# Kernel optimization log

Hardware: AMD Instinct MI355X
Metric: run time of the kernel (lower is better)

## Reference

```python
import jax, jax.numpy as jnp
import numpy as np

NUM_NODES = 100000
EMBED_DIM = 128
COMP_DIM = 64
T = 8
NSUB = 50000


def layer_norm(x, g, b, eps=1e-5):
    mu = jnp.mean(x, axis=-1, keepdims=True)
    var = jnp.mean((x - mu) ** 2, axis=-1, keepdims=True)
    return (x - mu) * jax.lax.rsqrt(var + eps) * g + b


def setup_inputs() -> dict:
    key = jax.random.key(0)
    ks = jax.random.split(key, 12)
    D, C = EMBED_DIM, COMP_DIM
    s = lambda n: 1.0 / np.sqrt(n)
    return {
        "x": jax.random.normal(ks[0], (T * NSUB, D), dtype=jnp.float32),
        "indices": jax.random.randint(ks[1], (T, NSUB), 0, NUM_NODES, dtype=jnp.int64),
        "bd": jax.random.normal(ks[2], (NUM_NODES, D), dtype=jnp.float32),
        "ln_d_g": jnp.ones((D,), jnp.float32), "ln_d_b": jnp.zeros((D,), jnp.float32),
        "Wd1": jax.random.normal(ks[3], (D, 2 * D), jnp.float32) * s(D),
        "bd1": jnp.zeros((2 * D,), jnp.float32),
        "Wd2": jax.random.normal(ks[4], (2 * D, C), jnp.float32) * s(2 * D),
        "bd2": jnp.zeros((C,), jnp.float32),
        "ln_u_g": jnp.ones((C,), jnp.float32), "ln_u_b": jnp.zeros((C,), jnp.float32),
        "Wu1": jax.random.normal(ks[5], (C, 2 * C), jnp.float32) * s(C),
        "bu1": jnp.zeros((2 * C,), jnp.float32),
        "Wu2": jax.random.normal(ks[6], (2 * C, D), jnp.float32) * s(2 * C),
        "bu2": jnp.zeros((D,), jnp.float32),
    }


def reference(x, indices, bd, ln_d_g, ln_d_b, Wd1, bd1, Wd2, bd2,
              ln_u_g, ln_u_b, Wu1, bu1, Wu2, bu2):
    # _to_entire: per-timestep scatter-add of subnode feats into full node table
    x3 = x.reshape(T, NSUB, EMBED_DIM)  # [T, Nsub, D]
    scattered = jax.vmap(
        lambda xt, it: jax.ops.segment_sum(xt, it, num_segments=NUM_NODES)
    )(x3, indices)  # [T, num_nodes, D]
    inp = scattered + bd[None]  # ta + bd (use_bd=True)
    h = layer_norm(inp, ln_d_g, ln_d_b)
    # mlp_d: Linear -> GELU -> Dropout(eval=identity) -> Linear
    h = jax.nn.gelu(h @ Wd1 + bd1, approximate=False) @ Wd2 + bd2  # [T, num_nodes, C]
    # _from_entire: gather activated rows per timestep, then LN + mlp_u
    gathered = jax.vmap(lambda ht, it: ht[it])(h, indices)  # [T, Nsub, C]
    g = gathered.reshape(T * NSUB, COMP_DIM)
    u = layer_norm(g, ln_u_g, ln_u_b)
    out = jax.nn.gelu(u @ Wu1 + bu1, approximate=False) @ Wu2 + bu2  # [T*Nsub, D]
    return out
```

## Files before the change

kernel.cpp:

```cpp
#include <hip/hip_runtime.h>
#include <math.h>

#define NN 100000
#define DD 128
#define CC 64
#define TT 8
#define NS 50000
#define G8 8
#define MAXS 391
#define MAXS_B 196
#define T1MAX (G8 * MAXS)
#define T2MAX (G8 * MAXS_B)
#define L2CAP 25000

typedef __attribute__((ext_vector_type(4))) float f32x4;
typedef __attribute__((ext_vector_type(8))) short bf16x8;
typedef unsigned short ushort_t;

__device__ __forceinline__ short f2bf(float f) {
    union { float f; unsigned u; } v; v.f = f;
    unsigned r = v.u + 0x7fffu + ((v.u >> 16) & 1u);
    return (short)(r >> 16);
}
__device__ __forceinline__ unsigned pk_bf16(float lo, float hi) {
    unsigned r;
    asm("v_cvt_pk_bf16_f32 %0, %1, %2" : "=v"(r) : "v"(lo), "v"(hi));
    return r;
}
__device__ __forceinline__ float gelu(float x) {
    float t = x + 0.044715f * x * x * x;
    return x / (1.0f + __expf(-1.5957691216f * t));
}

__global__ void prep_all(const float* __restrict__ Wd1, const float* __restrict__ Wd2,
                         const float* __restrict__ Wu1, const float* __restrict__ Wu2,
                         short* __restrict__ pW1, short* __restrict__ pW2,
                         short* __restrict__ pW3, short* __restrict__ pW4) {
    int b = blockIdx.x;
    const float* W; short* dst; int KSTEPS, total, N, s0;
    if (b < 16)      { W = Wd1; dst = pW1; KSTEPS = 4; total = 4096; N = 256; s0 = b * 256; }
    else if (b < 24) { W = Wd2; dst = pW2; KSTEPS = 8; total = 2048; N = 64;  s0 = (b - 16) * 256; }
    else if (b < 28) { W = Wu1; dst = pW3; KSTEPS = 2; total = 1024; N = 128; s0 = (b - 24) * 256; }
    else             { W = Wu2; dst = pW4; KSTEPS = 4; total = 2048; N = 128; s0 = (b - 28) * 256; }
    int s = s0 + threadIdx.x;
    if (s >= total) return;
    int lane = s & 63;
    int ks = (s >> 6) % KSTEPS;
    int n = s / (64 * KSTEPS);
    int kb = ks * 32 + (lane >> 4) * 8;
    int col = n * 16 + (lane & 15);
    bf16x8 o;
    #pragma unroll
    for (int j = 0; j < 8; ++j) o[j] = f2bf(W[(size_t)(kb + j) * N + col]);
    *(bf16x8*)(dst + (size_t)s * 8) = o;
}

__global__ void flagfill_kernel(const int* __restrict__ idx, int* __restrict__ pernode,
                                ushort_t* __restrict__ bucket) {
    int i = blockIdx.x * 256 + threadIdx.x;
    if (i >= G8 * NS) return;
    int g = i / NS, s = i - g * NS;
    int node = idx[i];
    int p = atomicAdd(&pernode[node * 8 + g], 1);
    if (p < 16) bucket[((size_t)node * 8 + g) * 16 + p] = (ushort_t)s;
}

__global__ void compact2_kernel(const int* __restrict__ idx, const int* __restrict__ pernode,
                                int* __restrict__ list1, int* __restrict__ cnts1,
                                int* __restrict__ list2, int* __restrict__ cnts2) {
    int g = blockIdx.y;
    int i = blockIdx.x * 256 + threadIdx.x;
    int lane = threadIdx.x & 63;
    bool a1 = false;
    if (i < NS) {
        int nd = idx[(size_t)g * NS + i];
        a1 = (pernode[nd * 8 + g] == 1);
    }
    unsigned long long m1 = __ballot(a1);
    int r1 = __popcll(m1 & ((1ull << lane) - 1ull));
    int c1 = __popcll(m1);
    int b1 = 0;
    if (lane == 0 && c1 > 0) b1 = atomicAdd(&cnts1[g], c1);
    b1 = __shfl(b1, 0);
    if (a1) list1[(size_t)g * NS + b1 + r1] = i;
    bool a2 = (i < NN) && (pernode[i * 8 + g] >= 2);
    unsigned long long m2 = __ballot(a2);
    int r2 = __popcll(m2 & ((1ull << lane) - 1ull));
    int c2 = __popcll(m2);
    int b2 = 0;
    if (lane == 0 && c2 > 0) b2 = atomicAdd(&cnts2[g], c2);
    b2 = __shfl(b2, 0);
    if (a2) list2[(size_t)g * L2CAP + b2 + r2] = i;
}

__device__ __forceinline__ void ln_d_pack(
    const float (&v)[32], int kgrp,
    const float* __restrict__ lndg, const float* __restrict__ lndb, bf16x8 (&afr)[4]) {
    float s1 = 0.f;
    #pragma unroll
    for (int j = 0; j < 32; ++j) s1 += v[j];
    s1 += __shfl_xor(s1, 16); s1 += __shfl_xor(s1, 32);
    float mu = s1 * 0.0078125f;
    float s2 = 0.f;
    #pragma unroll
    for (int j = 0; j < 32; ++j) { float d = v[j] - mu; s2 += d * d; }
    s2 += __shfl_xor(s2, 16); s2 += __shfl_xor(s2, 32);
    float rs = rsqrtf(s2 * 0.0078125f + 1e-5f);
    union U8 { bf16x8 v8; unsigned u[4]; };
    const float* gp = lndg + kgrp * 8;
    const float* bbp = lndb + kgrp * 8;
    #pragma unroll
    for (int ks = 0; ks < 4; ++ks) {
        float4 g0 = *(const float4*)(gp + ks * 32);
        float4 g1 = *(const float4*)(gp + ks * 32 + 4);
        float4 c0 = *(const float4*)(bbp + ks * 32);
        float4 c1 = *(const float4*)(bbp + ks * 32 + 4);
        U8 t;
        t.u[0] = pk_bf16((v[ks*8+0]-mu)*rs*g0.x + c0.x, (v[ks*8+1]-mu)*rs*g0.y + c0.y);
        t.u[1] = pk_bf16((v[ks*8+2]-mu)*rs*g0.z + c0.z, (v[ks*8+3]-mu)*rs*g0.w + c0.w);
        t.u[2] = pk_bf16((v[ks*8+4]-mu)*rs*g1.x + c1.x, (v[ks*8+5]-mu)*rs*g1.y + c1.y);
        t.u[3] = pk_bf16((v[ks*8+6]-mu)*rs*g1.z + c1.z, (v[ks*8+7]-mu)*rs*g1.w + c1.w);
        afr[ks] = t.v8;
    }
}

__device__ __forceinline__ void mlp_core(
    const bf16x8 (&afr)[4], short* myb, int arow, int kgrp,
    const short* sW1, const short* sW2, const short* __restrict__ pW3, const short* sW4,
    const float* __restrict__ bd1, const float* __restrict__ bd2,
    const float* __restrict__ lnug, const float* __restrict__ lnub,
    const float* __restrict__ bu1, f32x4 (&acc4)[8]) {
    const int lane = kgrp * 16 + arow;
    f32x4 acc2[4];
    #pragma unroll
    for (int n = 0; n < 4; ++n) acc2[n] = (f32x4){0.f, 0.f, 0.f, 0.f};
    for (int ks2 = 0; ks2 < 8; ++ks2) {
        f32x4 a1v[2];
        a1v[0] = (f32x4){0.f, 0.f, 0.f, 0.f};
        a1v[1] = (f32x4){0.f, 0.f, 0.f, 0.f};
        #pragma unroll
        for (int ks1 = 0; ks1 < 4; ++ks1) {
            #pragma unroll
            for (int p = 0; p < 2; ++p) {
                bf16x8 bf = *(const bf16x8*)(sW1 + (size_t)((((2 * ks2 + p) << 2) | ks1) * 64 + lane) * 8);
                a1v[p] = __builtin_amdgcn_mfma_f32_16x16x32_bf16(afr[ks1], bf, a1v[p], 0, 0, 0);
            }
        }
        #pragma unroll
        for (int p = 0; p < 2; ++p) {
            float bias = bd1[(2 * ks2 + p) * 16 + arow];
            #pragma unroll
            for (int rr = 0; rr < 4; ++rr) {
                float vv = gelu(a1v[p][rr] + bias);
                int row = kgrp * 4 + rr;
                int byte = row * 64 + (((p * 16 + arow) * 2) ^ ((row & 3) << 4));
                myb[byte >> 1] = f2bf(vv);
            }
        }
        bf16x8 af2 = *(const bf16x8*)(myb + ((arow * 64 + ((kgrp * 16) ^ ((arow & 3) << 4))) >> 1));
        #pragma unroll
        for (int n2 = 0; n2 < 4; ++n2) {
            bf16x8 bf = *(const bf16x8*)(sW2 + (size_t)(((n2 << 3) | ks2) * 64 + lane) * 8);
            acc2[n2] = __builtin_amdgcn_mfma_f32_16x16x32_bf16(af2, bf, acc2[n2], 0, 0, 0);
        }
    }
    float hv[4][4];
    #pragma unroll
    for (int n2 = 0; n2 < 4; ++n2)
        #pragma unroll
        for (int rr = 0; rr < 4; ++rr)
            hv[n2][rr] = acc2[n2][rr] + bd2[n2 * 16 + arow];
    #pragma unroll
    for (int rr = 0; rr < 4; ++rr) {
        float sr = hv[0][rr] + hv[1][rr] + hv[2][rr] + hv[3][rr];
        sr += __shfl_xor(sr, 1); sr += __shfl_xor(sr, 2);
        sr += __shfl_xor(sr, 4); sr += __shfl_xor(sr, 8);
        float mu_u = sr * 0.015625f;
        float sq = 0.f;
        #pragma unroll
        for (int n2 = 0; n2 < 4; ++n2) { float d = hv[n2][rr] - mu_u; sq += d * d; }
        sq += __shfl_xor(sq, 1); sq += __shfl_xor(sq, 2);
        sq += __shfl_xor(sq, 4); sq += __shfl_xor(sq, 8);
        float rs_u = rsqrtf(sq * 0.015625f + 1e-5f);
        #pragma unroll
        for (int n2 = 0; n2 < 4; ++n2) {
            int cidx = n2 * 16 + arow;
            float nv = (hv[n2][rr] - mu_u) * rs_u * lnug[cidx] + lnub[cidx];
            int row = kgrp * 4 + rr;
            int byte = row * 128 + ((cidx * 2) ^ ((row & 7) << 4));
            myb[byte >> 1] = f2bf(nv);
        }
    }
    bf16x8 af3[2];
    #pragma unroll
    for (int ks3 = 0; ks3 < 2; ++ks3)
        af3[ks3] = *(const bf16x8*)(myb + ((arow * 128 + ((ks3 * 64 + kgrp * 16) ^ ((arow & 7) << 4))) >> 1));
    #pragma unroll
    for (int n = 0; n < 8; ++n) acc4[n] = (f32x4){0.f, 0.f, 0.f, 0.f};
    #pragma unroll
    for (int half = 0; half < 2; ++half) {
        f32x4 a3[4];
        #pragma unroll
        for (int n = 0; n < 4; ++n) a3[n] = (f32x4){0.f, 0.f, 0.f, 0.f};
        #pragma unroll
        for (int ks3 = 0; ks3 < 2; ++ks3) {
            #pragma unroll
            for (int n3h = 0; n3h < 4; ++n3h) {
                int n3 = half * 4 + n3h;
                bf16x8 bf = *(const bf16x8*)(pW3 + (size_t)(((n3 << 1) | ks3) * 64 + lane) * 8);
                a3[n3h] = __builtin_amdgcn_mfma_f32_16x16x32_bf16(af3[ks3], bf, a3[n3h], 0, 0, 0);
            }
        }
        #pragma unroll
        for (int n3h = 0; n3h < 4; ++n3h) {
            float bias = bu1[(half * 4 + n3h) * 16 + arow];
            #pragma unroll
            for (int rr = 0; rr < 4; ++rr) {
                float vv = gelu(a3[n3h][rr] + bias);
                int row = kgrp * 4 + rr;
                int byte = row * 128 + (((n3h * 16 + arow) * 2) ^ ((row & 7) << 4));
                myb[byte >> 1] = f2bf(vv);
            }
        }
        #pragma unroll
        for (int k4 = 0; k4 < 2; ++k4) {
            bf16x8 afu = *(const bf16x8*)(myb + ((arow * 128 + ((k4 * 64 + kgrp * 16) ^ ((arow & 7) << 4))) >> 1));
            #pragma unroll
            for (int n4 = 0; n4 < 8; ++n4) {
                bf16x8 bf = *(const bf16x8*)(sW4 + (size_t)(((n4 << 2) | (half * 2 + k4)) * 64 + lane) * 8);
                acc4[n4] = __builtin_amdgcn_mfma_f32_16x16x32_bf16(afu, bf, acc4[n4], 0, 0, 0);
            }
        }
    }
}

__global__ __launch_bounds__(512, 2) void fused_kernel(
    const float* __restrict__ x, const int* __restrict__ idx,
    const float* __restrict__ bd,
    const float* __restrict__ lndg, const float* __restrict__ lndb,
    const short* __restrict__ pW1, const short* __restrict__ pW2,
    const short* __restrict__ pW3, const short* __restrict__ pW4,
    const float* __restrict__ bd1, const float* __restrict__ bd2,
    const float* __restrict__ lnug, const float* __restrict__ lnub,
    const float* __restrict__ bu1, const float* __restrict__ bu2,
    const int* __restrict__ list1, const int* __restrict__ cnts1,
    const int* __restrict__ list2, const int* __restrict__ cnts2,
    const int* __restrict__ pernode, const ushort_t* __restrict__ bucket,
    float* __restrict__ out) {
    __shared__ short sW1[4096 * 8];
    __shared__ short sW2[2048 * 8];
    __shared__ short sW4[2048 * 8];
    __shared__ short sBuf[8][1024];

    const int tid = threadIdx.x;
    for (int s = tid; s < 4096; s += 512)
        *(bf16x8*)(sW1 + s * 8) = *(const bf16x8*)(pW1 + (size_t)s * 8);
    for (int s = tid; s < 2048; s += 512)
        *(bf16x8*)(sW2 + s * 8) = *(const bf16x8*)(pW2 + (size_t)s * 8);
    for (int s = tid; s < 2048; s += 512)
        *(bf16x8*)(sW4 + s * 8) = *(const bf16x8*)(pW4 + (size_t)s * 8);
    __syncthreads();

    const int wave = tid >> 6, lane = tid & 63;
    short* myb = sBuf[wave];
    float* mf = (float*)myb;
    const int arow = lane & 15;
    const int kgrp = lane >> 4;
    const int q32 = lane >> 5, c32 = lane & 31;

    for (int w = blockIdx.x; w < T1MAX + T2MAX; w += gridDim.x) {
        if (w < T1MAX) {
            const int g = w & 7, strip = w >> 3;
            const int n1g = cnts1[g];
            const int row0 = strip * 128 + wave * 16;
            if (row0 >= n1g) continue;
            const float* x_g = x + (size_t)g * NS * DD;
            float* out_g = out + (size_t)g * NS * DD;
            const int gi = row0 + arow;
            const int s_val = list1[(size_t)g * NS + (gi < n1g ? gi : n1g - 1)];
            const int node = idx[(size_t)g * NS + s_val];
            float v[32];
            {
                const float* xp = x_g + (size_t)s_val * DD + kgrp * 8;
                const float* bp = bd + (size_t)node * DD + kgrp * 8;
                #pragma unroll
                for (int ks = 0; ks < 4; ++ks) {
                    float4 a0 = *(const float4*)(xp + ks * 32);
                    float4 a1 = *(const float4*)(xp + ks * 32 + 4);
                    float4 b0 = *(const float4*)(bp + ks * 32);
                    float4 b1 = *(const float4*)(bp + ks * 32 + 4);
                    v[ks*8+0] = a0.x + b0.x; v[ks*8+1] = a0.y + b0.y;
                    v[ks*8+2] = a0.z + b0.z; v[ks*8+3] = a0.w + b0.w;
                    v[ks*8+4] = a1.x + b1.x; v[ks*8+5] = a1.y + b1.y;
                    v[ks*8+6] = a1.z + b1.z; v[ks*8+7] = a1.w + b1.w;
                }
            }
            bf16x8 afr[4];
            ln_d_pack(v, kgrp, lndg, lndb, afr);
            f32x4 acc4[8];
            mlp_core(afr, myb, arow, kgrp, sW1, sW2, pW3, sW4,
                     bd1, bd2, lnug, lnub, bu1, acc4);
            #pragma unroll
            for (int rr = 0; rr < 4; ++rr) {
                #pragma unroll
                for (int n4 = 0; n4 < 8; ++n4) {
                    int col = n4 * 16 + arow;
                    int blk = (col >> 2) ^ kgrp;
                    mf[kgrp * 128 + blk * 4 + (col & 3)] = acc4[n4][rr] + bu2[col];
                }
                #pragma unroll
                for (int pair = 0; pair < 2; ++pair) {
                    int slot = pair * 2 + q32;
                    int src = slot * 4 + rr;
                    int s2v = __shfl(s_val, src);
                    float4 val = *(const float4*)(mf + slot * 128 + ((c32 ^ slot) * 4));
                    if (row0 + src < n1g)
                        *(float4*)(out_g + (size_t)s2v * DD + c32 * 4) = val;
                }
            }
        } else {
            const int w2 = w - T1MAX;
            const int g = w2 & 7, strip = w2 >> 3;
            const int n2g = cnts2[g];
            const int row0 = strip * 128 + wave * 16;
            if (row0 >= n2g) continue;
            const float* x_g = x + (size_t)g * NS * DD;
            float* out_g = out + (size_t)g * NS * DD;
            const int gi = row0 + arow;
            const int node = list2[(size_t)g * L2CAP + (gi < n2g ? gi : n2g - 1)];
            const int c = pernode[node * 8 + g];
            const int4 p8 = *(const int4*)(bucket + ((size_t)node * 8 + g) * 16);
            const int pr0 = p8.x & 0xffff, pr1 = ((unsigned)p8.x) >> 16;
            float v[32];
            {
                const float* bp = bd + (size_t)node * DD + kgrp * 8;
                const float* xq0 = x_g + (size_t)pr0 * DD + kgrp * 8;
                const float* xq1 = x_g + (size_t)pr1 * DD + kgrp * 8;
                #pragma unroll
                for (int ks = 0; ks < 4; ++ks) {
                    float4 b0 = *(const float4*)(bp + ks * 32);
                    float4 b1 = *(const float4*)(bp + ks * 32 + 4);
                    float4 a0 = *(const float4*)(xq0 + ks * 32);
                    float4 a1 = *(const float4*)(xq0 + ks * 32 + 4);
                    float4 d0 = *(const float4*)(xq1 + ks * 32);
                    float4 d1 = *(const float4*)(xq1 + ks * 32 + 4);
                    v[ks*8+0] = b0.x + a0.x + d0.x;
                    v[ks*8+1] = b0.y + a0.y + d0.y;
                    v[ks*8+2] = b0.z + a0.z + d0.z;
                    v[ks*8+3] = b0.w + a0.w + d0.w;
                    v[ks*8+4] = b1.x + a1.x + d1.x;
                    v[ks*8+5] = b1.y + a1.y + d1.y;
                    v[ks*8+6] = b1.z + a1.z + d1.z;
                    v[ks*8+7] = b1.w + a1.w + d1.w;
                }
            }
            if (__any(c > 2)) {
                const int pr2 = p8.y & 0xffff, pr3 = ((unsigned)p8.y) >> 16;
                const float* xq2 = x_g + (size_t)((c > 2) ? pr2 : pr0) * DD + kgrp * 8;
                const float* xq3 = x_g + (size_t)((c > 3) ? pr3 : pr0) * DD + kgrp * 8;
                const float m2 = (c > 2) ? 1.f : 0.f;
                const float m3 = (c > 3) ? 1.f : 0.f;
                #pragma unroll
                for (int ks = 0; ks < 4; ++ks) {
                    float4 a0 = *(const float4*)(xq2 + ks * 32);
                    float4 a1 = *(const float4*)(xq2 + ks * 32 + 4);
                    float4 d0 = *(const float4*)(xq3 + ks * 32);
                    float4 d1 = *(const float4*)(xq3 + ks * 32 + 4);
                    v[ks*8+0] = fmaf(m3, d0.x, fmaf(m2, a0.x, v[ks*8+0]));
                    v[ks*8+1] = fmaf(m3, d0.y, fmaf(m2, a0.y, v[ks*8+1]));
                    v[ks*8+2] = fmaf(m3, d0.z, fmaf(m2, a0.z, v[ks*8+2]));
                    v[ks*8+3] = fmaf(m3, d0.w, fmaf(m2, a0.w, v[ks*8+3]));
                    v[ks*8+4] = fmaf(m3, d1.x, fmaf(m2, a1.x, v[ks*8+4]));
                    v[ks*8+5] = fmaf(m3, d1.y, fmaf(m2, a1.y, v[ks*8+5]));
                    v[ks*8+6] = fmaf(m3, d1.z, fmaf(m2, a1.z, v[ks*8+6]));
                    v[ks*8+7] = fmaf(m3, d1.w, fmaf(m2, a1.w, v[ks*8+7]));
                }
            }
            if (__any(c > 4)) {
                const ushort_t* bt = bucket + ((size_t)node * 8 + g) * 16;
                for (int j = 4; j < 16; j += 2) {
                    if (!__any(c > j)) break;
                    const int pa = (j < c) ? bt[j] : pr0;
                    const int pb = (j + 1 < c) ? bt[j + 1] : pr0;
                    const float ma = (j < c) ? 1.f : 0.f;
                    const float mb = (j + 1 < c) ? 1.f : 0.f;
                    const float* xqa = x_g + (size_t)pa * DD + kgrp * 8;
                    const float* xqb = x_g + (size_t)pb * DD + kgrp * 8;
                    #pragma unroll
                    for (int ks = 0; ks < 4; ++ks) {
                        float4 a0 = *(const float4*)(xqa + ks * 32);
                        float4 a1 = *(const float4*)(xqa + ks * 32 + 4);
                        float4 d0 = *(const float4*)(xqb + ks * 32);
                        float4 d1 = *(const float4*)(xqb + ks * 32 + 4);
                        v[ks*8+0] = fmaf(mb, d0.x, fmaf(ma, a0.x, v[ks*8+0]));
                        v[ks*8+1] = fmaf(mb, d0.y, fmaf(ma, a0.y, v[ks*8+1]));
                        v[ks*8+2] = fmaf(mb, d0.z, fmaf(ma, a0.z, v[ks*8+2]));
                        v[ks*8+3] = fmaf(mb, d0.w, fmaf(ma, a0.w, v[ks*8+3]));
                        v[ks*8+4] = fmaf(mb, d1.x, fmaf(ma, a1.x, v[ks*8+4]));
                        v[ks*8+5] = fmaf(mb, d1.y, fmaf(ma, a1.y, v[ks*8+5]));
                        v[ks*8+6] = fmaf(mb, d1.z, fmaf(ma, a1.z, v[ks*8+6]));
                        v[ks*8+7] = fmaf(mb, d1.w, fmaf(ma, a1.w, v[ks*8+7]));
                    }
                }
            }
            bf16x8 afr[4];
            ln_d_pack(v, kgrp, lndg, lndb, afr);
            f32x4 acc4[8];
            mlp_core(afr, myb, arow, kgrp, sW1, sW2, pW3, sW4,
                     bd1, bd2, lnug, lnub, bu1, acc4);
            #pragma unroll
            for (int rr = 0; rr < 4; ++rr) {
                #pragma unroll
                for (int n4 = 0; n4 < 8; ++n4) {
                    int col = n4 * 16 + arow;
                    int blk = (col >> 2) ^ kgrp;
                    mf[kgrp * 128 + blk * 4 + (col & 3)] = acc4[n4][rr] + bu2[col];
                }
                #pragma unroll
                for (int pair = 0; pair < 2; ++pair) {
                    int slot = pair * 2 + q32;
                    int src = slot * 4 + rr;
                    int c2 = __shfl(c, src);
                    if (row0 + src >= n2g) c2 = 0;
                    unsigned u0 = (unsigned)__shfl(p8.x, src);
                    unsigned u1 = (unsigned)__shfl(p8.y, src);
                    unsigned u2 = (unsigned)__shfl(p8.z, src);
                    unsigned u3 = (unsigned)__shfl(p8.w, src);
                    float4 val = *(const float4*)(mf + slot * 128 + ((c32 ^ slot) * 4));
                    if (c2 > 0) *(float4*)(out_g + (size_t)(u0 & 0xffff) * DD + c32 * 4) = val;
                    if (c2 > 1) *(float4*)(out_g + (size_t)(u0 >> 16) * DD + c32 * 4) = val;
                    if (c2 > 2) *(float4*)(out_g + (size_t)(u1 & 0xffff) * DD + c32 * 4) = val;
                    if (c2 > 3) *(float4*)(out_g + (size_t)(u1 >> 16) * DD + c32 * 4) = val;
                    if (__any(c2 > 4)) {
                        if (c2 > 4) *(float4*)(out_g + (size_t)(u2 & 0xffff) * DD + c32 * 4) = val;
                        if (c2 > 5) *(float4*)(out_g + (size_t)(u2 >> 16) * DD + c32 * 4) = val;
                        if (c2 > 6) *(float4*)(out_g + (size_t)(u3 & 0xffff) * DD + c32 * 4) = val;
                        if (c2 > 7) *(float4*)(out_g + (size_t)(u3 >> 16) * DD + c32 * 4) = val;
                    }
                    if (__any(c2 > 8)) {
                        int nd2 = __shfl(node, src);
                        const ushort_t* bt = bucket + ((size_t)nd2 * 8 + g) * 16;
                        for (int j = 8; j < 16; ++j) {
                            if (!__any(j < c2)) break;
                            if (j < c2)
                                *(float4*)(out_g + (size_t)bt[j] * DD + c32 * 4) = val;
                        }
                    }
                }
            }
        }
    }
}

extern "C" void kernel_launch(void* const* d_in, const int* in_sizes, int n_in,
                              void* d_out, int out_size, void* d_ws, size_t ws_size,
                              hipStream_t stream) {
    const float* x       = (const float*)d_in[0];
    const int*   indices = (const int*)d_in[1];
    const float* bd      = (const float*)d_in[2];
    const float* ln_d_g  = (const float*)d_in[3];
    const float* ln_d_b  = (const float*)d_in[4];
    const float* Wd1     = (const float*)d_in[5];
    const float* bd1     = (const float*)d_in[6];
    const float* Wd2     = (const float*)d_in[7];
    const float* bd2     = (const float*)d_in[8];
    const float* ln_u_g  = (const float*)d_in[9];
    const float* ln_u_b  = (const float*)d_in[10];
    const float* Wu1     = (const float*)d_in[11];
    const float* bu1     = (const float*)d_in[12];
    const float* Wu2     = (const float*)d_in[13];
    const float* bu2     = (const float*)d_in[14];
    float* out = (float*)d_out;

    char* ws = (char*)d_ws;
    size_t o = 0;
    auto alloc_b = [&](size_t bytes) { char* p = ws + o; o = (o + bytes + 255) & ~(size_t)255; return p; };
    int*      pernode = (int*)alloc_b((size_t)NN * 8 * 4);
    int*      cnts1   = (int*)alloc_b(8 * 4);
    int*      cnts2   = (int*)alloc_b(8 * 4);
    size_t zero_bytes = (size_t)((char*)cnts2 - (char*)pernode) + 256;
    int*      list1   = (int*)alloc_b((size_t)8 * NS * 4);
    int*      list2   = (int*)alloc_b((size_t)8 * L2CAP * 4);
    ushort_t* bucket  = (ushort_t*)alloc_b((size_t)NN * 8 * 16 * 2);
    short*    pW1     = (short*)alloc_b((size_t)4096 * 16);
    short*    pW2     = (short*)alloc_b((size_t)2048 * 16);
    short*    pW3     = (short*)alloc_b((size_t)1024 * 16);
    short*    pW4     = (short*)alloc_b((size_t)2048 * 16);

    hipMemsetAsync(pernode, 0, zero_bytes, stream);

    prep_all<<<36, 256, 0, stream>>>(Wd1, Wd2, Wu1, Wu2, pW1, pW2, pW3, pW4);
    flagfill_kernel<<<(G8 * NS + 255) / 256, 256, 0, stream>>>(indices, pernode, bucket);
    compact2_kernel<<<dim3((NN + 255) / 256, G8), 256, 0, stream>>>(indices, pernode,
                                                                    list1, cnts1,
                                                                    list2, cnts2);
    fused_kernel<<<256, 512, 0, stream>>>(x, indices, bd, ln_d_g, ln_d_b,
                                          pW1, pW2, pW3, pW4,
                                          bd1, bd2, ln_u_g, ln_u_b, bu1, bu2,
                                          list1, cnts1, list2, cnts2,
                                          pernode, bucket, out);
}
```

Before: 421.2 us.

## Fold memset into prep kernel, store node with list1, unify fused paths

The separate hipMemsetAsync is replaced by extra blocks in prep_all that zero the pernode/count region with int4 stores, which removes one launch. list1 now stores (position, node) pairs, so the fused kernel no longer does a dependent idx gather per row. The two segment branches in the fused kernel are merged into one code path, with the MLP and LN shared, which shrinks code size and may ease register pressure. The cost is a larger list1 buffer and some extra branching on segA inside the merged path.

```diff
diff --git a/kernel.cpp b/kernel.cpp
--- a/kernel.cpp
+++ b/kernel.cpp
@@ -12,6 +12,7 @@
 #define T1MAX (G8 * MAXS)
 #define T2MAX (G8 * MAXS_B)
 #define L2CAP 25000
+#define ZINT4 200032
 
 typedef __attribute__((ext_vector_type(4))) float f32x4;
 typedef __attribute__((ext_vector_type(8))) short bf16x8;
@@ -35,8 +36,14 @@
 __global__ void prep_all(const float* __restrict__ Wd1, const float* __restrict__ Wd2,
                          const float* __restrict__ Wu1, const float* __restrict__ Wu2,
                          short* __restrict__ pW1, short* __restrict__ pW2,
-                         short* __restrict__ pW3, short* __restrict__ pW4) {
+                         short* __restrict__ pW3, short* __restrict__ pW4,
+                         int4* __restrict__ zbase) {
     int b = blockIdx.x;
+    if (b >= 36) {
+        int i = (b - 36) * 256 + threadIdx.x;
+        if (i < ZINT4) zbase[i] = (int4){0, 0, 0, 0};
+        return;
+    }
     const float* W; short* dst; int KSTEPS, total, N, s0;
     if (b < 16)      { W = Wd1; dst = pW1; KSTEPS = 4; total = 4096; N = 256; s0 = b * 256; }
     else if (b < 24) { W = Wd2; dst = pW2; KSTEPS = 8; total = 2048; N = 64;  s0 = (b - 16) * 256; }
@@ -66,15 +73,16 @@
 }
 
 __global__ void compact2_kernel(const int* __restrict__ idx, const int* __restrict__ pernode,
-                                int* __restrict__ list1, int* __restrict__ cnts1,
+                                int2* __restrict__ list1, int* __restrict__ cnts1,
                                 int* __restrict__ list2, int* __restrict__ cnts2) {
     int g = blockIdx.y;
     int i = blockIdx.x * 256 + threadIdx.x;
     int lane = threadIdx.x & 63;
     bool a1 = false;
+    int nd1 = 0;
     if (i < NS) {
-        int nd = idx[(size_t)g * NS + i];
-        a1 = (pernode[nd * 8 + g] == 1);
+        nd1 = idx[(size_t)g * NS + i];
+        a1 = (pernode[nd1 * 8 + g] == 1);
     }
     unsigned long long m1 = __ballot(a1);
     int r1 = __popcll(m1 & ((1ull << lane) - 1ull));
@@ -82,7 +90,7 @@
     int b1 = 0;
     if (lane == 0 && c1 > 0) b1 = atomicAdd(&cnts1[g], c1);
     b1 = __shfl(b1, 0);
-    if (a1) list1[(size_t)g * NS + b1 + r1] = i;
+    if (a1) list1[(size_t)g * NS + b1 + r1] = (int2){i, nd1};
     bool a2 = (i < NN) && (pernode[i * 8 + g] >= 2);
     unsigned long long m2 = __ballot(a2);
     int r2 = __popcll(m2 & ((1ull << lane) - 1ull));
@@ -235,15 +243,14 @@
 }
 
 __global__ __launch_bounds__(512, 2) void fused_kernel(
-    const float* __restrict__ x, const int* __restrict__ idx,
-    const float* __restrict__ bd,
+    const float* __restrict__ x, const float* __restrict__ bd,
     const float* __restrict__ lndg, const float* __restrict__ lndb,
     const short* __restrict__ pW1, const short* __restrict__ pW2,
     const short* __restrict__ pW3, const short* __restrict__ pW4,
     const float* __restrict__ bd1, const float* __restrict__ bd2,
     const float* __restrict__ lnug, const float* __restrict__ lnub,
     const float* __restrict__ bu1, const float* __restrict__ bu2,
-    const int* __restrict__ list1, const int* __restrict__ cnts1,
+    const int2* __restrict__ list1, const int* __restrict__ cnts1,
     const int* __restrict__ list2, const int* __restrict__ cnts2,
     const int* __restrict__ pernode, const ushort_t* __restrict__ bucket,
     float* __restrict__ out) {
@@ -269,95 +276,66 @@
     const int q32 = lane >> 5, c32 = lane & 31;
 
     for (int w = blockIdx.x; w < T1MAX + T2MAX; w += gridDim.x) {
-        if (w < T1MAX) {
-            const int g = w & 7, strip = w >> 3;
-            const int n1g = cnts1[g];
-            const int row0 = strip * 128 + wave * 16;
-            if (row0 >= n1g) continue;
-            const float* x_g = x + (size_t)g * NS * DD;
-            float* out_g = out + (size_t)g * NS * DD;
-            const int gi = row0 + arow;
-            const int s_val = list1[(size_t)g * NS + (gi < n1g ? gi : n1g - 1)];
-            const int node = idx[(size_t)g * NS + s_val];
-            float v[32];
+        const bool segA = w < T1MAX;
+        int g, row0, nrow;
+        if (segA) {
+            g = w & 7; row0 = (w >> 3) * 128 + wave * 16; nrow = cnts1[g];
+        } else {
+            int w2 = w - T1MAX;
+            g = w2 & 7; row0 = (w2 >> 3) * 128 + wave * 16; nrow = cnts2[g];
+        }
+        if (row0 >= nrow) continue;
+        const float* x_g = x + (size_t)g * NS * DD;
+        float* out_g = out + (size_t)g * NS * DD;
+        const int gi = row0 + arow;
+        const int gidx = gi < nrow ? gi : nrow - 1;
+
+        int node, c = 1, pos0;
+        int4 p8 = (int4){0, 0, 0, 0};
+        if (segA) {
+            int2 pn = list1[(size_t)g * NS + gidx];
+            pos0 = pn.x; node = pn.y;
+        } else {
+            node = list2[(size_t)g * L2CAP + gidx];
+            c = pernode[node * 8 + g];
+            p8 = *(const int4*)(bucket + ((size_t)node * 8 + g) * 16);
+            pos0 = p8.x & 0xffff;
+        }
+
+        float v[32];
+        {
+            const float* xp = x_g + (size_t)pos0 * DD + kgrp * 8;
+            const float* bp = bd + (size_t)node * DD + kgrp * 8;
+            #pragma unroll
+            for (int ks = 0; ks < 4; ++ks) {
+                float4 a0 = *(const float4*)(xp + ks * 32);
+                float4 a1 = *(const float4*)(xp + ks * 32 + 4);
+                float4 b0 = *(const float4*)(bp + ks * 32);
+                float4 b1 = *(const float4*)(bp + ks * 32 + 4);
+                v[ks*8+0] = a0.x + b0.x; v[ks*8+1] = a0.y + b0.y;
+                v[ks*8+2] = a0.z + b0.z; v[ks*8+3] = a0.w + b0.w;
+                v[ks*8+4] = a1.x + b1.x; v[ks*8+5] = a1.y + b1.y;
+                v[ks*8+6] = a1.z + b1.z; v[ks*8+7] = a1.w + b1.w;
+            }
+        }
+        if (!segA) {
+            const int pr1 = ((unsigned)p8.x) >> 16;
             {
-                const float* xp = x_g + (size_t)s_val * DD + kgrp * 8;
-                const float* bp = bd + (size_t)node * DD + kgrp * 8;
-                #pragma unroll
-                for (int ks = 0; ks < 4; ++ks) {
-                    float4 a0 = *(const float4*)(xp + ks * 32);
-                    float4 a1 = *(const float4*)(xp + ks * 32 + 4);
-                    float4 b0 = *(const float4*)(bp + ks * 32);
-                    float4 b1 = *(const float4*)(bp + ks * 32 + 4);
-                    v[ks*8+0] = a0.x + b0.x; v[ks*8+1] = a0.y + b0.y;
-                    v[ks*8+2] = a0.z + b0.z; v[ks*8+3] = a0.w + b0.w;
-                    v[ks*8+4] = a1.x + b1.x; v[ks*8+5] = a1.y + b1.y;
-                    v[ks*8+6] = a1.z + b1.z; v[ks*8+7] = a1.w + b1.w;
-                }
-            }
-            bf16x8 afr[4];
-            ln_d_pack(v, kgrp, lndg, lndb, afr);
-            f32x4 acc4[8];
-            mlp_core(afr, myb, arow, kgrp, sW1, sW2, pW3, sW4,
-                     bd1, bd2, lnug, lnub, bu1, acc4);
-            #pragma unroll
-            for (int rr = 0; rr < 4; ++rr) {
-                #pragma unroll
-                for (int n4 = 0; n4 < 8; ++n4) {
-                    int col = n4 * 16 + arow;
-                    int blk = (col >> 2) ^ kgrp;
-                    mf[kgrp * 128 + blk * 4 + (col & 3)] = acc4[n4][rr] + bu2[col];
-                }
-                #pragma unroll
-                for (int pair = 0; pair < 2; ++pair) {
-                    int slot = pair * 2 + q32;
-                    int src = slot * 4 + rr;
-                    int s2v = __shfl(s_val, src);
-                    float4 val = *(const float4*)(mf + slot * 128 + ((c32 ^ slot) * 4));
-                    if (row0 + src < n1g)
-                        *(float4*)(out_g + (size_t)s2v * DD + c32 * 4) = val;
-                }
-            }
-        } else {
-            const int w2 = w - T1MAX;
-            const int g = w2 & 7, strip = w2 >> 3;
-            const int n2g = cnts2[g];
-            const int row0 = strip * 128 + wave * 16;
-            if (row0 >= n2g) continue;
-            const float* x_g = x + (size_t)g * NS * DD;
-            float* out_g = out + (size_t)g * NS * DD;
-            const int gi = row0 + arow;
-            const int node = list2[(size_t)g * L2CAP + (gi < n2g ? gi : n2g - 1)];
-            const int c = pernode[node * 8 + g];
-            const int4 p8 = *(const int4*)(bucket + ((size_t)node * 8 + g) * 16);
-            const int pr0 = p8.x & 0xffff, pr1 = ((unsigned)p8.x) >> 16;
-            float v[32];
-            {
-                const float* bp = bd + (size_t)node * DD + kgrp * 8;
-                const float* xq0 = x_g + (size_t)pr0 * DD + kgrp * 8;
                 const float* xq1 = x_g + (size_t)pr1 * DD + kgrp * 8;
                 #pragma unroll
                 for (int ks = 0; ks < 4; ++ks) {
-                    float4 b0 = *(const float4*)(bp + ks * 32);
-                    float4 b1 = *(const float4*)(bp + ks * 32 + 4);
-                    float4 a0 = *(const float4*)(xq0 + ks * 32);
-                    float4 a1 = *(const float4*)(xq0 + ks * 32 + 4);
                     float4 d0 = *(const float4*)(xq1 + ks * 32);
                     float4 d1 = *(const float4*)(xq1 + ks * 32 + 4);
-                    v[ks*8+0] = b0.x + a0.x + d0.x;
-                    v[ks*8+1] = b0.y + a0.y + d0.y;
-                    v[ks*8+2] = b0.z + a0.z + d0.z;
-                    v[ks*8+3] = b0.w + a0.w + d0.w;
-                    v[ks*8+4] = b1.x + a1.x + d1.x;
-                    v[ks*8+5] = b1.y + a1.y + d1.y;
-                    v[ks*8+6] = b1.z + a1.z + d1.z;
-                    v[ks*8+7] = b1.w + a1.w + d1.w;
+                    v[ks*8+0] += d0.x; v[ks*8+1] += d0.y;
+                    v[ks*8+2] += d0.z; v[ks*8+3] += d0.w;
+                    v[ks*8+4] += d1.x; v[ks*8+5] += d1.y;
+                    v[ks*8+6] += d1.z; v[ks*8+7] += d1.w;
                 }
             }
             if (__any(c > 2)) {
                 const int pr2 = p8.y & 0xffff, pr3 = ((unsigned)p8.y) >> 16;
-                const float* xq2 = x_g + (size_t)((c > 2) ? pr2 : pr0) * DD + kgrp * 8;
-                const float* xq3 = x_g + (size_t)((c > 3) ? pr3 : pr0) * DD + kgrp * 8;
+                const float* xq2 = x_g + (size_t)((c > 2) ? pr2 : pos0) * DD + kgrp * 8;
+                const float* xq3 = x_g + (size_t)((c > 3) ? pr3 : pos0) * DD + kgrp * 8;
                 const float m2 = (c > 2) ? 1.f : 0.f;
                 const float m3 = (c > 3) ? 1.f : 0.f;
                 #pragma unroll
@@ -380,8 +358,8 @@
                 const ushort_t* bt = bucket + ((size_t)node * 8 + g) * 16;
                 for (int j = 4; j < 16; j += 2) {
                     if (!__any(c > j)) break;
-                    const int pa = (j < c) ? bt[j] : pr0;
-                    const int pb = (j + 1 < c) ? bt[j + 1] : pr0;
+                    const int pa = (j < c) ? bt[j] : pos0;
+                    const int pb = (j + 1 < c) ? bt[j + 1] : pos0;
                     const float ma = (j < c) ? 1.f : 0.f;
                     const float mb = (j + 1 < c) ? 1.f : 0.f;
                     const float* xqa = x_g + (size_t)pa * DD + kgrp * 8;
@@ -403,30 +381,39 @@
                     }
                 }
             }
-            bf16x8 afr[4];
-            ln_d_pack(v, kgrp, lndg, lndb, afr);
-            f32x4 acc4[8];
-            mlp_core(afr, myb, arow, kgrp, sW1, sW2, pW3, sW4,
-                     bd1, bd2, lnug, lnub, bu1, acc4);
-            #pragma unroll
-            for (int rr = 0; rr < 4; ++rr) {
-                #pragma unroll
-                for (int n4 = 0; n4 < 8; ++n4) {
-                    int col = n4 * 16 + arow;
-                    int blk = (col >> 2) ^ kgrp;
-                    mf[kgrp * 128 + blk * 4 + (col & 3)] = acc4[n4][rr] + bu2[col];
-                }
-                #pragma unroll
-                for (int pair = 0; pair < 2; ++pair) {
-                    int slot = pair * 2 + q32;
-                    int src = slot * 4 + rr;
+        }
+
+        bf16x8 afr[4];
+        ln_d_pack(v, kgrp, lndg, lndb, afr);
+        f32x4 acc4[8];
+        mlp_core(afr, myb, arow, kgrp, sW1, sW2, pW3, sW4,
+                 bd1, bd2, lnug, lnub, bu1, acc4);
+
+        #pragma unroll
+        for (int rr = 0; rr < 4; ++rr) {
+            #pragma unroll
+            for (int n4 = 0; n4 < 8; ++n4) {
+                int col = n4 * 16 + arow;
+                int blk = (col >> 2) ^ kgrp;
+                mf[kgrp * 128 + blk * 4 + (col & 3)] = acc4[n4][rr] + bu2[col];
+            }
+            #pragma unroll
+            for (int pair = 0; pair < 2; ++pair) {
+                int slot = pair * 2 + q32;
+                int src = slot * 4 + rr;
+                bool valid = (row0 + src) < nrow;
+                float4 val = *(const float4*)(mf + slot * 128 + ((c32 ^ slot) * 4));
+                if (segA) {
+                    int p0v = __shfl(pos0, src);
+                    if (valid)
+                        *(float4*)(out_g + (size_t)p0v * DD + c32 * 4) = val;
+                } else {
                     int c2 = __shfl(c, src);
-                    if (row0 + src >= n2g) c2 = 0;
+                    if (!valid) c2 = 0;
                     unsigned u0 = (unsigned)__shfl(p8.x, src);
                     unsigned u1 = (unsigned)__shfl(p8.y, src);
                     unsigned u2 = (unsigned)__shfl(p8.z, src);
                     unsigned u3 = (unsigned)__shfl(p8.w, src);
-                    float4 val = *(const float4*)(mf + slot * 128 + ((c32 ^ slot) * 4));
                     if (c2 > 0) *(float4*)(out_g + (size_t)(u0 & 0xffff) * DD + c32 * 4) = val;
                     if (c2 > 1) *(float4*)(out_g + (size_t)(u0 >> 16) * DD + c32 * 4) = val;
                     if (c2 > 2) *(float4*)(out_g + (size_t)(u1 & 0xffff) * DD + c32 * 4) = val;
@@ -478,8 +465,7 @@
     int*      pernode = (int*)alloc_b((size_t)NN * 8 * 4);
     int*      cnts1   = (int*)alloc_b(8 * 4);
     int*      cnts2   = (int*)alloc_b(8 * 4);
-    size_t zero_bytes = (size_t)((char*)cnts2 - (char*)pernode) + 256;
-    int*      list1   = (int*)alloc_b((size_t)8 * NS * 4);
+    int2*     list1   = (int2*)alloc_b((size_t)8 * NS * 8);
     int*      list2   = (int*)alloc_b((size_t)8 * L2CAP * 4);
     ushort_t* bucket  = (ushort_t*)alloc_b((size_t)NN * 8 * 16 * 2);
     short*    pW1     = (short*)alloc_b((size_t)4096 * 16);
@@ -487,14 +473,14 @@
     short*    pW3     = (short*)alloc_b((size_t)1024 * 16);
     short*    pW4     = (short*)alloc_b((size_t)2048 * 16);
 
-    hipMemsetAsync(pernode, 0, zero_bytes, stream);
-
-    prep_all<<<36, 256, 0, stream>>>(Wd1, Wd2, Wu1, Wu2, pW1, pW2, pW3, pW4);
+    prep_all<<<36 + (ZINT4 + 255) / 256, 256, 0, stream>>>(Wd1, Wd2, Wu1, Wu2,
+                                                           pW1, pW2, pW3, pW4,
+                                                           (int4*)pernode);
     flagfill_kernel<<<(G8 * NS + 255) / 256, 256, 0, stream>>>(indices, pernode, bucket);
     compact2_kernel<<<dim3((NN + 255) / 256, G8), 256, 0, stream>>>(indices, pernode,
                                                                     list1, cnts1,
                                                                     list2, cnts2);
-    fused_kernel<<<256, 512, 0, stream>>>(x, indices, bd, ln_d_g, ln_d_b,
+    fused_kernel<<<256, 512, 0, stream>>>(x, bd, ln_d_g, ln_d_b,
                                           pW1, pW2, pW3, pW4,
                                           bd1, bd2, ln_u_g, ln_u_b, bu1, bu2,
                                           list1, cnts1, list2, cnts2,
```

After: 421.2 us. No clear change (+0.0%).
